# Kernel optimization log

Hardware: AMD Instinct MI355X
Metric: run time of the kernel (lower is better)

## Reference

```python
import jax, jax.numpy as jnp
import numpy as np

HEADS = 8
OUT_CH = 128
DIMH_V = 16      # out_channels // heads
DIMH_QK = 8      # dim_head_v // 2
DIM = 128        # attention axis length == init dim
QKV_CH = 256     # heads * (dim_head_v + 2*dim_head_qk) == 2*out_channels
F_QR, F_KR, F_SV, F_SVE = 0.3, 0.3, 0.5, 0.3
BN_EPS = 1e-5


def _bn(x, gamma, beta, axes):
    # BatchNorm in training mode: per-channel (axis=1) batch statistics.
    mean = jnp.mean(x, axis=axes, keepdims=True)
    var = jnp.var(x, axis=axes, keepdims=True)
    xhat = (x - mean) * jax.lax.rsqrt(var + BN_EPS)
    shape = [1] * x.ndim
    shape[1] = -1
    return xhat * gamma.reshape(shape) + beta.reshape(shape)


def setup_inputs() -> dict:
    key = jax.random.key(0)
    ks = jax.random.split(key, 3)
    x = jax.random.normal(ks[0], (8, 128, 64, 128), dtype=jnp.float32)
    w_qkv = jax.random.normal(ks[1], (QKV_CH, 128), dtype=jnp.float32) * 0.05
    relative = jax.random.normal(ks[2], (2 * DIMH_V, 2 * DIM - 1), dtype=jnp.float32) * np.sqrt(1.0 / DIMH_V)
    ones = lambda c: jnp.ones((c,), jnp.float32)
    zeros = lambda c: jnp.zeros((c,), jnp.float32)
    return {
        "x": x, "w_qkv": w_qkv,
        "g1": ones(QKV_CH), "b1": zeros(QKV_CH),
        "g2": ones(QKV_CH), "b2": zeros(QKV_CH),
        "gs": ones(3 * HEADS), "bs": zeros(3 * HEADS),
        "go": ones(2 * OUT_CH), "bo": zeros(2 * OUT_CH),
        "relative": relative,
    }


def reference(x, w_qkv, g1, b1, g2, b2, gs, bs, go, bo, relative):
    N, C, Wax, H = x.shape  # flag=True: permute (0,2,1,3)
    xb = jnp.transpose(x, (0, 2, 1, 3)).reshape(N * Wax, C, H)

    # conv1x1 (no bias) + BN, then bn_qkv
    qkv = jnp.einsum('bch,oc->boh', xb, w_qkv)
    qkv = _bn(qkv, g1, b1, (0, 2))
    qkv = _bn(qkv, g2, b2, (0, 2))

    qkv = qkv.reshape(N * Wax, HEADS, 2 * DIMH_V, H)
    q = qkv[:, :, :DIMH_QK]                      # [b,g,8,H]
    k = qkv[:, :, DIMH_QK:2 * DIMH_QK]           # [b,g,8,H]
    v = qkv[:, :, 2 * DIMH_QK:]                  # [b,g,16,H]

    # gather relative embeddings: index[i,j] = i - j + H - 1
    idx = jnp.arange(H)[:, None] - jnp.arange(H)[None, :] + H - 1
    emb = relative[:, idx]                       # [32,H,H]
    q_emb = emb[:DIMH_QK]
    k_emb = emb[DIMH_QK:2 * DIMH_QK]
    v_emb = emb[2 * DIMH_QK:]

    qr = jnp.einsum('bgci,cij->bgij', q, q_emb) * F_QR
    kr = jnp.swapaxes(jnp.einsum('bgci,cij->bgij', k, k_emb), 2, 3) * F_KR
    qk = jnp.einsum('bgci,bgcj->bgij', q, k)

    stacked = jnp.concatenate([qk, qr, kr], axis=1)           # [b,3g,H,H]
    stacked = _bn(stacked, gs, bs, (0, 2, 3))
    stacked = stacked.reshape(N * Wax, 3, HEADS, H, H).sum(axis=1)
    sim = jax.nn.softmax(stacked, axis=3)                     # [b,g,H,H]

    sv = jnp.einsum('bgij,bgcj->bgci', sim, v) * F_SV
    sve = jnp.einsum('bgij,cij->bgci', sim, v_emb) * F_SVE
    so = jnp.concatenate([sv, sve], axis=-1).reshape(N * Wax, 2 * OUT_CH, H)
    so = _bn(so, go, bo, (0, 2))

    out = so.reshape(N, Wax, OUT_CH, 2, H).sum(axis=3)        # [N,W,Cout,H]
    return jnp.transpose(out, (0, 2, 1, 3))                   # flag=True
```

## Files before the change

### kernel.cpp

```cpp
#include <hip/hip_runtime.h>
#include <hip/hip_fp16.h>
#include <math.h>

#define B_TOT 512
#define CQKV  256
#define CIN   128
#define HLEN  128

static constexpr float F_QR = 0.3f, F_KR = 0.3f, F_SV = 0.5f, F_SVE = 0.3f;
static constexpr float EPS = 1e-5f;

typedef __attribute__((ext_vector_type(8))) short short8v;
typedef __attribute__((ext_vector_type(8))) _Float16 half8v;
typedef __attribute__((ext_vector_type(2))) _Float16 half2v;
typedef __attribute__((ext_vector_type(4))) float float4v;

#if __has_builtin(__builtin_amdgcn_fdot2)
#define HAVE_FDOT2 1
#endif

__device__ __forceinline__ unsigned short f2bf(float f) {
    unsigned u = __float_as_uint(f);
    unsigned r = u + 0x7fffu + ((u >> 16) & 1u);
    return (unsigned short)(r >> 16);
}
__device__ __forceinline__ unsigned short f2h(float f) {
    return __half_as_ushort(__float2half(f));
}

__global__ __launch_bounds__(256, 3) void k_qkv(const float* __restrict__ x,
                                                const float* __restrict__ w,
                                                float* __restrict__ qkv,
                                                double* __restrict__ accA) {
    __shared__ unsigned short As[64][136];
    __shared__ unsigned short Xs[256][64];
    __shared__ float wsum[64][2];
    int bid = blockIdx.x;
    int n   = bid >> 7;
    int sub = bid & 127;
    int mt  = sub >> 2;
    int ot  = sub & 3;
    int m0  = mt << 8;
    int o0  = ot << 6;
    int t   = threadIdx.x;

    if (t < 64) { wsum[t][0] = 0.f; wsum[t][1] = 0.f; }

#pragma unroll
    for (int it = 0; it < 8; ++it) {
        int idx = it * 256 + t;
        int o = idx >> 5, c4 = (idx & 31) << 2;
        float4 wv = *(const float4*)(w + (size_t)(o0 + o) * CIN + c4);
        As[o][c4 + 0] = f2bf(wv.x);
        As[o][c4 + 1] = f2bf(wv.y);
        As[o][c4 + 2] = f2bf(wv.z);
        As[o][c4 + 3] = f2bf(wv.w);
    }

    const float* xn = x + (size_t)n * CIN * 8192 + m0;

    int wv_ = t >> 6, l = t & 63;
    int lr = l & 15, lh = l >> 4;
    int mw = wv_ << 6;

    float4v acc[4][4];
#pragma unroll
    for (int a = 0; a < 4; ++a)
#pragma unroll
        for (int b2 = 0; b2 < 4; ++b2) acc[a][b2] = (float4v){0.f, 0.f, 0.f, 0.f};

    for (int s = 0; s < 2; ++s) {
        int c0 = s << 6;
        __syncthreads();
#pragma unroll
        for (int it = 0; it < 16; ++it) {
            int c  = (it << 2) + (t >> 6);
            int m4 = (t & 63) << 2;
            float4 xv = *(const float4*)(xn + (size_t)(c0 + c) * 8192 + m4);
            float vals[4] = {xv.x, xv.y, xv.z, xv.w};
#pragma unroll
            for (int j = 0; j < 4; ++j) {
                int m = m4 + j;
                int cs = (((c >> 3) ^ ((m >> 2) & 7)) << 3) | (c & 7);
                Xs[m][cs] = f2bf(vals[j]);
            }
        }
        __syncthreads();
#pragma unroll
        for (int ks = 0; ks < 2; ++ks) {
            short8v af[4], bf[4];
#pragma unroll
            for (int a = 0; a < 4; ++a)
                af[a] = *(const short8v*)&As[a * 16 + lr][c0 + ks * 32 + lh * 8];
#pragma unroll
            for (int b2 = 0; b2 < 4; ++b2) {
                int m  = mw + b2 * 16 + lr;
                int cb = (ks * 4 + lh) ^ ((m >> 2) & 7);
                bf[b2] = *(const short8v*)&Xs[m][cb << 3];
            }
#pragma unroll
            for (int a = 0; a < 4; ++a)
#pragma unroll
                for (int b2 = 0; b2 < 4; ++b2)
                    acc[a][b2] = __builtin_amdgcn_mfma_f32_16x16x32_bf16(
                        af[a], bf[b2], acc[a][b2], 0, 0, 0);
        }
    }

#pragma unroll
    for (int a = 0; a < 4; ++a) {
#pragma unroll
        for (int b2 = 0; b2 < 4; ++b2) {
            int m  = m0 + mw + b2 * 16 + lr;
            int bb = n * 64 + (m >> 7);
            int h  = m & 127;
#pragma unroll
            for (int r = 0; r < 4; ++r) {
                int o = o0 + a * 16 + lh * 4 + r;
                qkv[((size_t)bb * CQKV + o) * HLEN + h] = acc[a][b2][r];
            }
        }
    }

#pragma unroll
    for (int a = 0; a < 4; ++a) {
#pragma unroll
        for (int r = 0; r < 4; ++r) {
            float s = 0.f, ss = 0.f;
#pragma unroll
            for (int b2 = 0; b2 < 4; ++b2) {
                float v = acc[a][b2][r];
                s += v; ss += v * v;
            }
#pragma unroll
            for (int off = 1; off < 16; off <<= 1) {
                s  += __shfl_xor(s, off);
                ss += __shfl_xor(ss, off);
            }
            if (lr == 0) {
                int ol = a * 16 + lh * 4 + r;
                atomicAdd(&wsum[ol][0], s);
                atomicAdd(&wsum[ol][1], ss);
            }
        }
    }
    __syncthreads();
    if (t < 64) {
        atomicAdd(&accA[(size_t)(o0 + t) * 2 + 0], (double)wsum[t][0]);
        atomicAdd(&accA[(size_t)(o0 + t) * 2 + 1], (double)wsum[t][1]);
    }
}

__global__ void k_finA(const double* __restrict__ accA,
                       const float* __restrict__ g1, const float* __restrict__ g2,
                       const float* __restrict__ b2,
                       float* __restrict__ scaleA, float* __restrict__ shiftA) {
    int o = threadIdx.x;
    double cnt  = 65536.0;
    double mean = accA[o * 2] / cnt;
    double var  = accA[o * 2 + 1] / cnt - mean * mean;
    float r1 = rsqrtf((float)var + EPS);
    float v2 = g1[o] * g1[o] * (float)var * r1 * r1;
    float sc = g1[o] * g2[o] * r1 * rsqrtf(v2 + EPS);
    scaleA[o] = sc;
    shiftA[o] = b2[o] - (float)mean * sc;
}

__global__ void k_finF(const double* __restrict__ accF,
                       const float* __restrict__ go, const float* __restrict__ bo,
                       float* __restrict__ scaleF, float* __restrict__ shiftF) {
    int o = threadIdx.x;
    double cnt  = 65536.0;
    double mean = accF[o * 2] / cnt;
    double var  = accF[o * 2 + 1] / cnt - mean * mean;
    float sc = go[o] * rsqrtf((float)var + EPS);
    scaleF[o] = sc;
    shiftF[o] = bo[o] - (float)mean * sc;
}

__global__ __launch_bounds__(128) void k_tables(const float* __restrict__ rel,
                                                float* __restrict__ Rq, float* __restrict__ Rk,
                                                float* __restrict__ TqT, float* __restrict__ TkT) {
    int bid = blockIdx.x;
    int i = threadIdx.x;
    int p = bid & 63;
    int c = p >> 3, c2 = p & 7;
    const float* ra = (bid < 64) ? (rel + c * 255)  : (rel + (8 + c) * 255);
    const float* rb = (bid < 64) ? (rel + c2 * 255) : (rel + (8 + c2) * 255);
    float tacc = 0.f;
    for (int kk = 0; kk < 128; ++kk) tacc = fmaf(ra[i + kk], rb[i + kk], tacc);
    if (bid < 64) TqT[i * 64 + p] = tacc; else TkT[i * 64 + p] = tacc;
    if (c2 == 0) {
        float racc = 0.f;
        for (int kk = 0; kk < 128; ++kk) racc += ra[i + kk];
        if (bid < 64) Rq[c * 128 + i] = racc; else Rk[c * 128 + i] = racc;
    }
}

__global__ __launch_bounds__(256) void k_gram(const float* __restrict__ qkv,
                                              const float* __restrict__ scaleA,
                                              const float* __restrict__ shiftA,
                                              const float* __restrict__ Rq,
                                              const float* __restrict__ Rk,
                                              const float* __restrict__ TqT,
                                              const float* __restrict__ TkT,
                                              double* __restrict__ accS) {
    __shared__ float qs[8][132], ks[8][132];
    __shared__ float redA[4][64][4];
    __shared__ float redB[2][18];
    __shared__ float redC[3];
    int blk = blockIdx.x, b = blk >> 3, g = blk & 7;
    int t = threadIdx.x;
    for (int idx = t; idx < 2048; idx += 256) {
        int cc = idx >> 7, h = idx & 127, o = g * 32 + cc;
        float v = qkv[((size_t)b * CQKV + o) * HLEN + h] * scaleA[o] + shiftA[o];
        if (cc < 8) qs[cc][h] = v; else ks[cc - 8][h] = v;
    }
    __syncthreads();
    int lane = t & 63, wv = t >> 6;
    int c = lane >> 3, c2 = lane & 7;
    float gq = 0, gk = 0, tq = 0, tk = 0;
#pragma unroll 4
    for (int ii = 0; ii < 32; ++ii) {
        int i = wv * 32 + ii;
        float a = qs[c][i] * qs[c2][i];
        float e = ks[c][i] * ks[c2][i];
        gq += a; gk += e;
        tq = fmaf(a, TqT[i * 64 + lane], tq);
        tk = fmaf(e, TkT[i * 64 + lane], tk);
    }
    redA[wv][lane][0] = gq; redA[wv][lane][1] = gk;
    redA[wv][lane][2] = tq; redA[wv][lane][3] = tk;

    if (t < 128) {
        int h = t;
        float sqr = 0, skr = 0;
        float sq8l[8], sk8l[8];
#pragma unroll
        for (int c3 = 0; c3 < 8; ++c3) {
            float q0 = qs[c3][h], k0 = ks[c3][h];
            sq8l[c3] = q0; sk8l[c3] = k0;
            sqr = fmaf(q0, Rq[c3 * 128 + h], sqr);
            skr = fmaf(k0, Rk[c3 * 128 + h], skr);
        }
#pragma unroll
        for (int off = 1; off < 64; off <<= 1) {
            sqr += __shfl_xor(sqr, off);
            skr += __shfl_xor(skr, off);
#pragma unroll
            for (int c3 = 0; c3 < 8; ++c3) {
                sq8l[c3] += __shfl_xor(sq8l[c3], off);
                sk8l[c3] += __shfl_xor(sk8l[c3], off);
            }
        }
        if (lane == 0) {
            redB[wv][0] = sqr; redB[wv][1] = skr;
#pragma unroll
            for (int c3 = 0; c3 < 8; ++c3) {
                redB[wv][2 + c3]  = sq8l[c3];
                redB[wv][10 + c3] = sk8l[c3];
            }
        }
    }
    __syncthreads();
    if (t < 64) {
        float Gq = redA[0][t][0] + redA[1][t][0] + redA[2][t][0] + redA[3][t][0];
        float Gk = redA[0][t][1] + redA[1][t][1] + redA[2][t][1] + redA[3][t][1];
        float Tq = redA[0][t][2] + redA[1][t][2] + redA[2][t][2] + redA[3][t][2];
        float Tk = redA[0][t][3] + redA[1][t][3] + redA[2][t][3] + redA[3][t][3];
        float ssqk = Gq * Gk;
#pragma unroll
        for (int off = 1; off < 64; off <<= 1) {
            ssqk += __shfl_xor(ssqk, off);
            Tq   += __shfl_xor(Tq, off);
            Tk   += __shfl_xor(Tk, off);
        }
        if (t == 0) { redC[0] = ssqk; redC[1] = Tq; redC[2] = Tk; }
    }
    __syncthreads();
    if (t == 0) {
        float sqr = redB[0][0] + redB[1][0];
        float skr = redB[0][1] + redB[1][1];
        float sqk = 0;
#pragma unroll
        for (int c3 = 0; c3 < 8; ++c3)
            sqk += (redB[0][2 + c3] + redB[1][2 + c3]) * (redB[0][10 + c3] + redB[1][10 + c3]);
        atomicAdd(&accS[g * 2 + 0], (double)sqk);
        atomicAdd(&accS[g * 2 + 1], (double)redC[0]);
        atomicAdd(&accS[(8 + g) * 2 + 0], (double)(F_QR * sqr));
        atomicAdd(&accS[(8 + g) * 2 + 1], (double)(F_QR * F_QR * redC[1]));
        atomicAdd(&accS[(16 + g) * 2 + 0], (double)(F_KR * skr));
        atomicAdd(&accS[(16 + g) * 2 + 1], (double)(F_KR * F_KR * redC[2]));
    }
}

__global__ void k_sfin(const double* __restrict__ accS,
                       const float* __restrict__ gs, const float* __restrict__ bs,
                       float* __restrict__ scaleS, float* __restrict__ shiftS) {
    int c = threadIdx.x;
    if (c < 24) {
        double cnt  = 512.0 * 128.0 * 128.0;
        double mean = accS[c * 2] / cnt;
        double var  = accS[c * 2 + 1] / cnt - mean * mean;
        float sc = gs[c] * rsqrtf((float)var + EPS);
        scaleS[c] = sc;
        shiftS[c] = bs[c] - (float)mean * sc;
    }
}

__global__ __launch_bounds__(256, 4) void k_attn(const float* __restrict__ qkv,
                                                 const float* __restrict__ scaleA,
                                                 const float* __restrict__ shiftA,
                                                 const float* __restrict__ rel,
                                                 const float* __restrict__ scaleS,
                                                 const float* __restrict__ shiftS,
                                                 float* __restrict__ so,
                                                 double* __restrict__ accF) {
    __shared__ unsigned short qT[128][8];
    __shared__ unsigned short kF[128][8];
    __shared__ unsigned short vB[16][136];
    __shared__ unsigned short rqT[255][8];
    __shared__ unsigned short rkT[255][8];
    __shared__ unsigned short rvA[255][8];
    __shared__ unsigned short rvB[255][8];
    __shared__ float accL[32][2];
    int blk = blockIdx.x, b = blk >> 3, g = blk & 7;
    int t = threadIdx.x;
    if (t < 32) { accL[t][0] = 0.f; accL[t][1] = 0.f; }

#pragma unroll
    for (int it = 0; it < 4; ++it) {
        int idx = it * 256 + t;
        int cc = idx >> 5;
        int h4 = (idx & 31) << 2;
        int o = g * 32 + cc;
        float4 v4 = *(const float4*)(qkv + ((size_t)b * CQKV + o) * HLEN + h4);
        float sc = scaleA[o], sh = shiftA[o];
        float f0 = fmaf(v4.x, sc, sh), f1 = fmaf(v4.y, sc, sh);
        float f2 = fmaf(v4.z, sc, sh), f3 = fmaf(v4.w, sc, sh);
        if (cc < 8) {
            qT[h4][cc] = f2h(f0); qT[h4 + 1][cc] = f2h(f1);
            qT[h4 + 2][cc] = f2h(f2); qT[h4 + 3][cc] = f2h(f3);
        } else if (cc < 16) {
            kF[h4][cc - 8] = f2h(f0); kF[h4 + 1][cc - 8] = f2h(f1);
            kF[h4 + 2][cc - 8] = f2h(f2); kF[h4 + 3][cc - 8] = f2h(f3);
        } else {
            uint2 pk;
            pk.x = (unsigned)f2h(f0) | ((unsigned)f2h(f1) << 16);
            pk.y = (unsigned)f2h(f2) | ((unsigned)f2h(f3) << 16);
            *(uint2*)&vB[cc - 16][h4] = pk;
        }
    }
#pragma unroll
    for (int it = 0; it < 8; ++it) {
        int idx = it * 256 + t;
        if (idx < 2040) {
            float4 v = *(const float4*)(rel + (size_t)idx * 4);
            float vv[4] = {v.x, v.y, v.z, v.w};
#pragma unroll
            for (int e = 0; e < 4; ++e) {
                int lin = idx * 4 + e;
                int r = lin / 255;
                int d = lin - r * 255;
                unsigned short us = f2h(vv[e]);
                if (r < 8)       rqT[d][r] = us;
                else if (r < 16) rkT[d][r - 8] = us;
                else if (r < 24) rvA[d][r - 16] = us;
                else             rvB[d][r - 24] = us;
            }
        }
    }
    __syncthreads();

    float cA = scaleS[g], cB = F_QR * scaleS[8 + g], cC = F_KR * scaleS[16 + g];
    float shsum = shiftS[g] + shiftS[8 + g] + shiftS[16 + g];

    int w = t >> 6, l = t & 63;
    int lr = l & 15, lh = l >> 4;
    int i0 = w * 32 + lr;

    half2v q2[2][4];
    {
        uint4 qv0 = *(const uint4*)&qT[i0][0];
        uint4 qv1 = *(const uint4*)&qT[i0 + 16][0];
        q2[0][0] = *(half2v*)&qv0.x; q2[0][1] = *(half2v*)&qv0.y;
        q2[0][2] = *(half2v*)&qv0.z; q2[0][3] = *(half2v*)&qv0.w;
        q2[1][0] = *(half2v*)&qv1.x; q2[1][1] = *(half2v*)&qv1.y;
        q2[1][2] = *(half2v*)&qv1.z; q2[1][3] = *(half2v*)&qv1.w;
    }

    float p0[32], p1[32];
    float rm0 = -1e30f, rm1 = -1e30f;
#pragma unroll
    for (int ks = 0; ks < 4; ++ks) {
#pragma unroll
        for (int e = 0; e < 8; ++e) {
            int j = ks * 32 + lh * 8 + e;
            uint4 kv = *(const uint4*)&kF[j][0];
            half2v* k2p = (half2v*)&kv;
#pragma unroll
            for (int it2 = 0; it2 < 2; ++it2) {
                int i = i0 + it2 * 16;
                uint4 rq = *(const uint4*)&rqT[i - j + 127][0];
                uint4 rk = *(const uint4*)&rkT[j - i + 127][0];
                half2v* rq2p = (half2v*)&rq;
                half2v* rk2p = (half2v*)&rk;
#ifdef HAVE_FDOT2
                float qk = __builtin_amdgcn_fdot2(q2[it2][0], k2p[0],
                           __builtin_amdgcn_fdot2(q2[it2][1], k2p[1],
                           __builtin_amdgcn_fdot2(q2[it2][2], k2p[2],
                           __builtin_amdgcn_fdot2(q2[it2][3], k2p[3], 0.f, false), false), false), false);
                float qr = __builtin_amdgcn_fdot2(q2[it2][0], rq2p[0],
                           __builtin_amdgcn_fdot2(q2[it2][1], rq2p[1],
                           __builtin_amdgcn_fdot2(q2[it2][2], rq2p[2],
                           __builtin_amdgcn_fdot2(q2[it2][3], rq2p[3], 0.f, false), false), false), false);
                float kr = __builtin_amdgcn_fdot2(k2p[0], rk2p[0],
                           __builtin_amdgcn_fdot2(k2p[1], rk2p[1],
                           __builtin_amdgcn_fdot2(k2p[2], rk2p[2],
                           __builtin_amdgcn_fdot2(k2p[3], rk2p[3], 0.f, false), false), false), false);
#else
                __half2* qh = (__half2*)&q2[it2][0];
                __half2* kk2 = (__half2*)&kv;
                __half2* rq2 = (__half2*)&rq;
                __half2* rk2 = (__half2*)&rk;
                __half2 hqk = __hfma2(qh[0], kk2[0], __hfma2(qh[1], kk2[1],
                              __hfma2(qh[2], kk2[2], __hmul2(qh[3], kk2[3]))));
                __half2 hqr = __hfma2(qh[0], rq2[0], __hfma2(qh[1], rq2[1],
                              __hfma2(qh[2], rq2[2], __hmul2(qh[3], rq2[3]))));
                __half2 hkr = __hfma2(kk2[0], rk2[0], __hfma2(kk2[1], rk2[1],
                              __hfma2(kk2[2], rk2[2], __hmul2(kk2[3], rk2[3]))));
                float qk = __low2float(hqk) + __high2float(hqk);
                float qr = __low2float(hqr) + __high2float(hqr);
                float kr = __low2float(hkr) + __high2float(hkr);
#endif
                float s = fmaf(qk, cA, fmaf(qr, cB, fmaf(kr, cC, shsum)));
                if (it2 == 0) { p0[ks * 8 + e] = s; rm0 = fmaxf(rm0, s); }
                else          { p1[ks * 8 + e] = s; rm1 = fmaxf(rm1, s); }
            }
        }
    }
    rm0 = fmaxf(rm0, __shfl_xor(rm0, 16)); rm0 = fmaxf(rm0, __shfl_xor(rm0, 32));
    rm1 = fmaxf(rm1, __shfl_xor(rm1, 16)); rm1 = fmaxf(rm1, __shfl_xor(rm1, 32));
    float rs0 = 0.f, rs1 = 0.f;
#pragma unroll
    for (int kk = 0; kk < 32; ++kk) {
        p0[kk] = __expf(p0[kk] - rm0); rs0 += p0[kk];
        p1[kk] = __expf(p1[kk] - rm1); rs1 += p1[kk];
    }
    rs0 += __shfl_xor(rs0, 16); rs0 += __shfl_xor(rs0, 32);
    rs1 += __shfl_xor(rs1, 16); rs1 += __shfl_xor(rs1, 32);
    float rn0 = 1.f / rs0, rn1 = 1.f / rs1;

    __half2 accA2[8], accB2[8];
#pragma unroll
    for (int m = 0; m < 8; ++m) {
        accA2[m] = __floats2half2_rn(0.f, 0.f);
        accB2[m] = __floats2half2_rn(0.f, 0.f);
    }
#pragma unroll
    for (int ks = 0; ks < 4; ++ks) {
#pragma unroll
        for (int e = 0; e < 8; ++e) {
            int j = ks * 32 + lh * 8 + e;
            {
                int d = i0 - j + 127;
                __half2 p2 = __float2half2_rn(p0[ks * 8 + e]);
                uint4 ra = *(const uint4*)&rvA[d][0];
                uint4 rb = *(const uint4*)&rvB[d][0];
                __half2* ra2 = (__half2*)&ra;
                __half2* rb2 = (__half2*)&rb;
                accA2[0] = __hfma2(p2, ra2[0], accA2[0]);
                accA2[1] = __hfma2(p2, ra2[1], accA2[1]);
                accA2[2] = __hfma2(p2, ra2[2], accA2[2]);
                accA2[3] = __hfma2(p2, ra2[3], accA2[3]);
                accA2[4] = __hfma2(p2, rb2[0], accA2[4]);
                accA2[5] = __hfma2(p2, rb2[1], accA2[5]);
                accA2[6] = __hfma2(p2, rb2[2], accA2[6]);
                accA2[7] = __hfma2(p2, rb2[3], accA2[7]);
            }
            {
                int d = i0 + 16 - j + 127;
                __half2 p2 = __float2half2_rn(p1[ks * 8 + e]);
                uint4 ra = *(const uint4*)&rvA[d][0];
                uint4 rb = *(const uint4*)&rvB[d][0];
                __half2* ra2 = (__half2*)&ra;
                __half2* rb2 = (__half2*)&rb;
                accB2[0] = __hfma2(p2, ra2[0], accB2[0]);
                accB2[1] = __hfma2(p2, ra2[1], accB2[1]);
                accB2[2] = __hfma2(p2, ra2[2], accB2[2]);
                accB2[3] = __hfma2(p2, ra2[3], accB2[3]);
                accB2[4] = __hfma2(p2, rb2[0], accB2[4]);
                accB2[5] = __hfma2(p2, rb2[1], accB2[5]);
                accB2[6] = __hfma2(p2, rb2[2], accB2[6]);
                accB2[7] = __hfma2(p2, rb2[3], accB2[7]);
            }
        }
    }
#pragma unroll
    for (int m = 0; m < 8; ++m) {
        unsigned ua = *(unsigned*)&accA2[m];
        unsigned t1 = __shfl_xor(ua, 16);
        accA2[m] = __hadd2(accA2[m], *(__half2*)&t1);
        ua = *(unsigned*)&accA2[m];
        t1 = __shfl_xor(ua, 32);
        accA2[m] = __hadd2(accA2[m], *(__half2*)&t1);
        unsigned ub = *(unsigned*)&accB2[m];
        unsigned t2 = __shfl_xor(ub, 16);
        accB2[m] = __hadd2(accB2[m], *(__half2*)&t2);
        ub = *(unsigned*)&accB2[m];
        t2 = __shfl_xor(ub, 32);
        accB2[m] = __hadd2(accB2[m], *(__half2*)&t2);
    }
    {
        float sce0 = F_SVE * rn0, sce1 = F_SVE * rn1;
        float s_c[4], ss_c[4];
#pragma unroll
        for (int cc = 0; cc < 4; ++cc) {
            int c = lh * 4 + cc;
            __half2 ha = accA2[c >> 1];
            __half2 hb = accB2[c >> 1];
            float v0 = ((c & 1) ? __high2float(ha) : __low2float(ha)) * sce0;
            float v1 = ((c & 1) ? __high2float(hb) : __low2float(hb)) * sce1;
            size_t base = ((size_t)b * CQKV + g * 32 + 2 * c + 1) * HLEN;
            so[base + i0]      = v0;
            so[base + i0 + 16] = v1;
            s_c[cc]  = v0 + v1;
            ss_c[cc] = v0 * v0 + v1 * v1;
        }
#pragma unroll
        for (int off = 1; off < 16; off <<= 1) {
#pragma unroll
            for (int cc = 0; cc < 4; ++cc) {
                s_c[cc]  += __shfl_xor(s_c[cc], off);
                ss_c[cc] += __shfl_xor(ss_c[cc], off);
            }
        }
        if (lr == 0) {
#pragma unroll
            for (int cc = 0; cc < 4; ++cc) {
                int c = lh * 4 + cc;
                atomicAdd(&accL[2 * c + 1][0], s_c[cc]);
                atomicAdd(&accL[2 * c + 1][1], ss_c[cc]);
            }
        }
    }

    unsigned ph[32];
#pragma unroll
    for (int ks = 0; ks < 4; ++ks) {
#pragma unroll
        for (int e2 = 0; e2 < 4; ++e2) {
            __half2 h0 = __floats2half2_rn(p0[ks * 8 + 2 * e2] * rn0,
                                           p0[ks * 8 + 2 * e2 + 1] * rn0);
            __half2 h1 = __floats2half2_rn(p1[ks * 8 + 2 * e2] * rn1,
                                           p1[ks * 8 + 2 * e2 + 1] * rn1);
            ph[ks * 4 + e2]      = *(unsigned*)&h0;
            ph[16 + ks * 4 + e2] = *(unsigned*)&h1;
        }
    }

    {
        float s0 = 0.f, ss0 = 0.f;
#pragma unroll
        for (int it2 = 0; it2 < 2; ++it2) {
            int itile = w * 2 + it2;
            float4v acc = {0.f, 0.f, 0.f, 0.f};
#pragma unroll
            for (int ks = 0; ks < 4; ++ks) {
                half8v af = *(half8v*)&ph[it2 * 16 + ks * 4];
                half8v bf = *(const half8v*)&vB[lr][ks * 32 + lh * 8];
                acc = __builtin_amdgcn_mfma_f32_16x16x32_f16(af, bf, acc, 0, 0, 0);
            }
            int oc = g * 32 + 2 * lr;
            float* sop = so + ((size_t)b * CQKV + oc) * HLEN + itile * 16 + lh * 4;
            float4 outv;
            outv.x = acc[0] * F_SV; outv.y = acc[1] * F_SV;
            outv.z = acc[2] * F_SV; outv.w = acc[3] * F_SV;
            *(float4*)sop = outv;
            s0  += outv.x + outv.y + outv.z + outv.w;
            ss0 += outv.x * outv.x + outv.y * outv.y + outv.z * outv.z + outv.w * outv.w;
        }
        s0  += __shfl_xor(s0, 16);  s0  += __shfl_xor(s0, 32);
        ss0 += __shfl_xor(ss0, 16); ss0 += __shfl_xor(ss0, 32);
        if (lh == 0) {
            atomicAdd(&accL[2 * lr][0], s0);
            atomicAdd(&accL[2 * lr][1], ss0);
        }
    }
    __syncthreads();
    if (t < 32) {
        int o = g * 32 + t;
        atomicAdd(&accF[(size_t)o * 2 + 0], (double)accL[t][0]);
        atomicAdd(&accF[(size_t)o * 2 + 1], (double)accL[t][1]);
    }
}

__global__ __launch_bounds__(256) void k_out(const float* __restrict__ so,
                                             const float* __restrict__ scale,
                                             const float* __restrict__ shift,
                                             float* __restrict__ out) {
    int b = blockIdx.x, n = b >> 6, wi = b & 63;
    int t = threadIdx.x;
    int h4  = (t & 31) << 2;
    int oc0 = (t >> 5) << 4;
    for (int k = 0; k < 16; ++k) {
        int oc = oc0 + k;
        float4 v0 = *(const float4*)(so + ((size_t)b * CQKV + 2 * oc) * HLEN + h4);
        float4 v1 = *(const float4*)(so + ((size_t)b * CQKV + 2 * oc + 1) * HLEN + h4);
        float s0 = scale[2 * oc], f0 = shift[2 * oc];
        float s1 = scale[2 * oc + 1], f1 = shift[2 * oc + 1];
        float4 o4;
        o4.x = fmaf(v0.x, s0, f0) + fmaf(v1.x, s1, f1);
        o4.y = fmaf(v0.y, s0, f0) + fmaf(v1.y, s1, f1);
        o4.z = fmaf(v0.z, s0, f0) + fmaf(v1.z, s1, f1);
        o4.w = fmaf(v0.w, s0, f0) + fmaf(v1.w, s1, f1);
        *(float4*)(out + (((size_t)n * 128 + oc) * 64 + wi) * HLEN + h4) = o4;
    }
}

extern "C" void kernel_launch(void* const* d_in, const int* in_sizes, int n_in,
                              void* d_out, int out_size, void* d_ws, size_t ws_size,
                              hipStream_t stream) {
    const float* x   = (const float*)d_in[0];
    const float* w   = (const float*)d_in[1];
    const float* g1  = (const float*)d_in[2];
    const float* b1  = (const float*)d_in[3];
    const float* g2  = (const float*)d_in[4];
    const float* b2  = (const float*)d_in[5];
    const float* gs  = (const float*)d_in[6];
    const float* bs  = (const float*)d_in[7];
    const float* go  = (const float*)d_in[8];
    const float* bo  = (const float*)d_in[9];
    const float* rel = (const float*)d_in[10];
    float* out = (float*)d_out;

    float*  qkv    = (float*)d_ws;
    float*  so     = qkv + (size_t)16777216;
    double* accA   = (double*)(so + (size_t)16777216);
    double* accS   = accA + 512;
    double* accF   = accS + 48;
    float*  scaleA = (float*)(accF + 512);
    float*  shiftA = scaleA + 256;
    float*  scaleS = shiftA + 256;
    float*  shiftS = scaleS + 24;
    float*  scaleF = shiftS + 24;
    float*  shiftF = scaleF + 256;
    float*  Rq     = shiftF + 256;
    float*  Rk     = Rq + 1024;
    float*  TqT    = Rk + 1024;
    float*  TkT    = TqT + 8192;

    hipMemsetAsync(accA, 0, (512 + 48 + 512) * sizeof(double), stream);

    k_qkv<<<1024, 256, 0, stream>>>(x, w, qkv, accA);
    k_tables<<<128, 128, 0, stream>>>(rel, Rq, Rk, TqT, TkT);
    k_finA<<<1, 256, 0, stream>>>(accA, g1, g2, b2, scaleA, shiftA);
    k_gram<<<4096, 256, 0, stream>>>(qkv, scaleA, shiftA, Rq, Rk, TqT, TkT, accS);
    k_sfin<<<1, 32, 0, stream>>>(accS, gs, bs, scaleS, shiftS);
    k_attn<<<4096, 256, 0, stream>>>(qkv, scaleA, shiftA, rel, scaleS, shiftS, so, accF);
    k_finF<<<1, 256, 0, stream>>>(accF, go, bo, scaleF, shiftF);
    k_out<<<512, 256, 0, stream>>>(so, scaleF, shiftF, out);
}
```

Before: 313.4 us.

## Store qkv and attention-output intermediates in fp16 to halve memory traffic

Result: slower. 370.6 us (+18.2%).

```diff
diff --git a/kernel.cpp b/kernel.cpp
--- a/kernel.cpp
+++ b/kernel.cpp
@@ -30,7 +30,7 @@
 
 __global__ __launch_bounds__(256, 3) void k_qkv(const float* __restrict__ x,
                                                 const float* __restrict__ w,
-                                                float* __restrict__ qkv,
+                                                unsigned short* __restrict__ qkv,
                                                 double* __restrict__ accA) {
     __shared__ unsigned short As[64][136];
     __shared__ unsigned short Xs[256][64];
@@ -117,7 +117,7 @@
 #pragma unroll
             for (int r = 0; r < 4; ++r) {
                 int o = o0 + a * 16 + lh * 4 + r;
-                qkv[((size_t)bb * CQKV + o) * HLEN + h] = acc[a][b2][r];
+                qkv[((size_t)bb * CQKV + o) * HLEN + h] = f2h(acc[a][b2][r]);
             }
         }
     }
@@ -197,7 +197,7 @@
     }
 }
 
-__global__ __launch_bounds__(256) void k_gram(const float* __restrict__ qkv,
+__global__ __launch_bounds__(256) void k_gram(const unsigned short* __restrict__ qkv,
                                               const float* __restrict__ scaleA,
                                               const float* __restrict__ shiftA,
                                               const float* __restrict__ Rq,
@@ -213,7 +213,8 @@
     int t = threadIdx.x;
     for (int idx = t; idx < 2048; idx += 256) {
         int cc = idx >> 7, h = idx & 127, o = g * 32 + cc;
-        float v = qkv[((size_t)b * CQKV + o) * HLEN + h] * scaleA[o] + shiftA[o];
+        float raw = __half2float(__ushort_as_half(qkv[((size_t)b * CQKV + o) * HLEN + h]));
+        float v = raw * scaleA[o] + shiftA[o];
         if (cc < 8) qs[cc][h] = v; else ks[cc - 8][h] = v;
     }
     __syncthreads();
@@ -308,13 +309,13 @@
     }
 }
 
-__global__ __launch_bounds__(256, 4) void k_attn(const float* __restrict__ qkv,
+__global__ __launch_bounds__(256, 6) void k_attn(const unsigned short* __restrict__ qkv,
                                                  const float* __restrict__ scaleA,
                                                  const float* __restrict__ shiftA,
                                                  const float* __restrict__ rel,
                                                  const float* __restrict__ scaleS,
                                                  const float* __restrict__ shiftS,
-                                                 float* __restrict__ so,
+                                                 unsigned short* __restrict__ so,
                                                  double* __restrict__ accF) {
     __shared__ unsigned short qT[128][8];
     __shared__ unsigned short kF[128][8];
@@ -334,20 +335,24 @@
         int cc = idx >> 5;
         int h4 = (idx & 31) << 2;
         int o = g * 32 + cc;
-        float4 v4 = *(const float4*)(qkv + ((size_t)b * CQKV + o) * HLEN + h4);
-        float sc = scaleA[o], sh = shiftA[o];
-        float f0 = fmaf(v4.x, sc, sh), f1 = fmaf(v4.y, sc, sh);
-        float f2 = fmaf(v4.z, sc, sh), f3 = fmaf(v4.w, sc, sh);
+        uint2 v4 = *(const uint2*)(qkv + ((size_t)b * CQKV + o) * HLEN + h4);
+        __half2 sc2 = __float2half2_rn(scaleA[o]);
+        __half2 sh2 = __float2half2_rn(shiftA[o]);
+        __half2 va = __hfma2(*(__half2*)&v4.x, sc2, sh2);
+        __half2 vb2 = __hfma2(*(__half2*)&v4.y, sc2, sh2);
+        unsigned ua = *(unsigned*)&va, ub = *(unsigned*)&vb2;
         if (cc < 8) {
-            qT[h4][cc] = f2h(f0); qT[h4 + 1][cc] = f2h(f1);
-            qT[h4 + 2][cc] = f2h(f2); qT[h4 + 3][cc] = f2h(f3);
+            qT[h4][cc]     = (unsigned short)(ua & 0xffff);
+            qT[h4 + 1][cc] = (unsigned short)(ua >> 16);
+            qT[h4 + 2][cc] = (unsigned short)(ub & 0xffff);
+            qT[h4 + 3][cc] = (unsigned short)(ub >> 16);
         } else if (cc < 16) {
-            kF[h4][cc - 8] = f2h(f0); kF[h4 + 1][cc - 8] = f2h(f1);
-            kF[h4 + 2][cc - 8] = f2h(f2); kF[h4 + 3][cc - 8] = f2h(f3);
+            kF[h4][cc - 8]     = (unsigned short)(ua & 0xffff);
+            kF[h4 + 1][cc - 8] = (unsigned short)(ua >> 16);
+            kF[h4 + 2][cc - 8] = (unsigned short)(ub & 0xffff);
+            kF[h4 + 3][cc - 8] = (unsigned short)(ub >> 16);
         } else {
-            uint2 pk;
-            pk.x = (unsigned)f2h(f0) | ((unsigned)f2h(f1) << 16);
-            pk.y = (unsigned)f2h(f2) | ((unsigned)f2h(f3) << 16);
+            uint2 pk; pk.x = ua; pk.y = ub;
             *(uint2*)&vB[cc - 16][h4] = pk;
         }
     }
@@ -522,8 +527,8 @@
             float v0 = ((c & 1) ? __high2float(ha) : __low2float(ha)) * sce0;
             float v1 = ((c & 1) ? __high2float(hb) : __low2float(hb)) * sce1;
             size_t base = ((size_t)b * CQKV + g * 32 + 2 * c + 1) * HLEN;
-            so[base + i0]      = v0;
-            so[base + i0 + 16] = v1;
+            so[base + i0]      = f2h(v0);
+            so[base + i0 + 16] = f2h(v1);
             s_c[cc]  = v0 + v1;
             ss_c[cc] = v0 * v0 + v1 * v1;
         }
@@ -572,13 +577,14 @@
                 acc = __builtin_amdgcn_mfma_f32_16x16x32_f16(af, bf, acc, 0, 0, 0);
             }
             int oc = g * 32 + 2 * lr;
-            float* sop = so + ((size_t)b * CQKV + oc) * HLEN + itile * 16 + lh * 4;
-            float4 outv;
-            outv.x = acc[0] * F_SV; outv.y = acc[1] * F_SV;
-            outv.z = acc[2] * F_SV; outv.w = acc[3] * F_SV;
-            *(float4*)sop = outv;
-            s0  += outv.x + outv.y + outv.z + outv.w;
-            ss0 += outv.x * outv.x + outv.y * outv.y + outv.z * outv.z + outv.w * outv.w;
+            float ox = acc[0] * F_SV, oy = acc[1] * F_SV;
+            float oz = acc[2] * F_SV, ow = acc[3] * F_SV;
+            __half2 o01 = __floats2half2_rn(ox, oy);
+            __half2 o23 = __floats2half2_rn(oz, ow);
+            uint2 pk; pk.x = *(unsigned*)&o01; pk.y = *(unsigned*)&o23;
+            *(uint2*)(so + ((size_t)b * CQKV + oc) * HLEN + itile * 16 + lh * 4) = pk;
+            s0  += ox + oy + oz + ow;
+            ss0 += ox * ox + oy * oy + oz * oz + ow * ow;
         }
         s0  += __shfl_xor(s0, 16);  s0  += __shfl_xor(s0, 32);
         ss0 += __shfl_xor(ss0, 16); ss0 += __shfl_xor(ss0, 32);
@@ -595,7 +601,7 @@
     }
 }
 
-__global__ __launch_bounds__(256) void k_out(const float* __restrict__ so,
+__global__ __launch_bounds__(256) void k_out(const unsigned short* __restrict__ so,
                                              const float* __restrict__ scale,
                                              const float* __restrict__ shift,
                                              float* __restrict__ out) {
@@ -605,15 +611,17 @@
     int oc0 = (t >> 5) << 4;
     for (int k = 0; k < 16; ++k) {
         int oc = oc0 + k;
-        float4 v0 = *(const float4*)(so + ((size_t)b * CQKV + 2 * oc) * HLEN + h4);
-        float4 v1 = *(const float4*)(so + ((size_t)b * CQKV + 2 * oc + 1) * HLEN + h4);
+        uint2 u0 = *(const uint2*)(so + ((size_t)b * CQKV + 2 * oc) * HLEN + h4);
+        uint2 u1 = *(const uint2*)(so + ((size_t)b * CQKV + 2 * oc + 1) * HLEN + h4);
+        __half2 a0 = *(__half2*)&u0.x, a1 = *(__half2*)&u0.y;
+        __half2 b0 = *(__half2*)&u1.x, b1 = *(__half2*)&u1.y;
         float s0 = scale[2 * oc], f0 = shift[2 * oc];
         float s1 = scale[2 * oc + 1], f1 = shift[2 * oc + 1];
         float4 o4;
-        o4.x = fmaf(v0.x, s0, f0) + fmaf(v1.x, s1, f1);
-        o4.y = fmaf(v0.y, s0, f0) + fmaf(v1.y, s1, f1);
-        o4.z = fmaf(v0.z, s0, f0) + fmaf(v1.z, s1, f1);
-        o4.w = fmaf(v0.w, s0, f0) + fmaf(v1.w, s1, f1);
+        o4.x = fmaf(__low2float(a0),  s0, f0) + fmaf(__low2float(b0),  s1, f1);
+        o4.y = fmaf(__high2float(a0), s0, f0) + fmaf(__high2float(b0), s1, f1);
+        o4.z = fmaf(__low2float(a1),  s0, f0) + fmaf(__low2float(b1),  s1, f1);
+        o4.w = fmaf(__high2float(a1), s0, f0) + fmaf(__high2float(b1), s1, f1);
         *(float4*)(out + (((size_t)n * 128 + oc) * 64 + wi) * HLEN + h4) = o4;
     }
 }
@@ -634,8 +642,8 @@
     const float* rel = (const float*)d_in[10];
     float* out = (float*)d_out;
 
-    float*  qkv    = (float*)d_ws;
-    float*  so     = qkv + (size_t)16777216;
+    unsigned short* qkv = (unsigned short*)d_ws;
+    unsigned short* so  = qkv + (size_t)16777216;
     double* accA   = (double*)(so + (size_t)16777216);
     double* accS   = accA + 512;
     double* accF   = accS + 48;
```
